# Optimization experiments

Hardware: AMD Instinct MI355X
Metric: run time of the kernel (lower is better)

## Reference

```python
import jax, jax.numpy as jnp
import numpy as np

B, L, C, H, W = 4, 16, 64, 64, 64
F, NH, NB = 128, 2, 2


def _ln(x, w, b, eps=1e-5):
    # LayerNorm over last two dims (H, W), torch-style biased variance
    m = jnp.mean(x, axis=(-2, -1), keepdims=True)
    v = jnp.var(x, axis=(-2, -1), keepdims=True)
    return (x - m) * jax.lax.rsqrt(v + eps) * w + b


def _conv2d(x, w, b):
    # x: (N, Cin, H, W), w: (Cout, Cin, k, k) -- the (1,k,k) Conv3d acts per-frame
    y = jax.lax.conv_general_dilated(x, w, (1, 1), 'SAME',
                                     dimension_numbers=('NCHW', 'OIHW', 'NCHW'))
    return y + b[None, :, None, None]


def _combine(c1, c2):
    a1, b1 = c1
    a2, b2 = c2
    return a1 * a2, a2 * b1 + b2


def _forward(x, params_log, pBw_r, pBw_i, pBb_r, pBb_i, pCw_r, pCw_i, pCb_r, pCb_i,
             lru_ln_w, lru_ln_b, cin_w, cin_b, h3_w, h3_b, h1_w, h1_b,
             h_ln_w, h_ln_b, cout_w, cout_b, ffn_ln_w, ffn_ln_b):
    gelu = lambda t: jax.nn.gelu(t, approximate=False)
    Bsz, Ln, Cc, Hh, Ww = x.shape
    for i in range(NB):
        # ---- ConvLRULayer ----
        pl = params_log[i]
        nu = jnp.exp(pl[:Cc])            # (C, H)
        theta = jnp.exp(pl[Cc:2 * Cc])   # (C, H)
        gamma = jnp.exp(pl[2 * Cc:])     # (C, H)
        lamb = jnp.exp(jax.lax.complex(-nu, theta))  # (C, H) complex
        Bw = jax.lax.complex(pBw_r[i], pBw_i[i])
        Bb = jax.lax.complex(pBb_r[i], pBb_i[i])
        Cw = jax.lax.complex(pCw_r[i], pCw_i[i])
        Cb = jax.lax.complex(pCb_r[i], pCb_i[i])
        h = jnp.fft.fft2(x.astype(jnp.complex64), axes=(-2, -1))  # (B,L,C,H,W)
        h = jnp.einsum('blchw,oc->blohw', h, Bw) + Bb[None, None, :, None, None]
        h = h * gamma[None, None, :, :, None]
        # parallel scan: h[t] = lamb * h[t-1] + h[t] along L
        a = jnp.broadcast_to(lamb[None, None, :, :, None], (Bsz, Ln, Cc, Hh, 1))
        _, h = jax.lax.associative_scan(_combine, (a, h), axis=1)
        h = jnp.fft.ifft2(h, axes=(-2, -1))
        h = jnp.einsum('blchw,oc->blohw', h, Cw) + Cb[None, None, :, None, None]
        h = _ln(h.real, lru_ln_w[i], lru_ln_b[i])
        x = h + x
        # ---- FeedForward (all Conv3d have kernel 1 in L -> per-frame 2D) ----
        y = x.reshape(Bsz * Ln, Cc, Hh, Ww)
        y_ = gelu(_conv2d(y, cin_w[i], cin_b[i]))  # (B*L, F, H, W)
        for j in range(NH):
            t = gelu(_conv2d(y_, h3_w[i, j], h3_b[i, j]))
            t = gelu(jnp.einsum('nfhw,of->nohw', t, h1_w[i, j])
                     + h1_b[i, j][None, :, None, None])
            y_ = _ln(t, h_ln_w[i, j], h_ln_b[i, j]) + y_
        t = jnp.einsum('nfhw,of->nohw', y_, cout_w[i]) + cout_b[i][None, :, None, None]
        t = _ln(t, ffn_ln_w[i], ffn_ln_b[i])
        x = t.reshape(Bsz, Ln, Cc, Hh, Ww) + x
    return x


def setup_inputs() -> dict:
    key = jax.random.key(0)
    ks = jax.random.split(key, 16)
    x = jax.random.normal(ks[0], (B, L, C, H, W), jnp.float32)
    # LRU stability init (as in the torch module)
    r_min, r_max = 0.8, 0.99
    u1 = jax.random.uniform(ks[1], (NB, C, H), jnp.float32)
    u2 = jax.random.uniform(ks[2], (NB, C, H), jnp.float32)
    nu_log = jnp.log(-0.5 * jnp.log(u1 * (r_max ** 2 - r_min ** 2) + r_min ** 2))
    theta_log = jnp.log(u2 * 2.0 * np.pi)
    gamma_log = 0.5 * jnp.log(1.0 - jnp.exp(-2.0 * jnp.exp(nu_log)))
    params_log = jnp.concatenate([nu_log, theta_log, gamma_log], axis=1)  # (NB, 3C, H)

    def nrm(k, shape, fan_in):
        return jax.random.normal(k, shape, jnp.float32) / np.sqrt(fan_in)

    return dict(
        x=x, params_log=params_log,
        pBw_r=nrm(ks[3], (NB, C, C), C), pBw_i=jnp.zeros((NB, C, C), jnp.float32),
        pBb_r=jnp.zeros((NB, C), jnp.float32), pBb_i=jnp.zeros((NB, C), jnp.float32),
        pCw_r=nrm(ks[4], (NB, C, C), C), pCw_i=jnp.zeros((NB, C, C), jnp.float32),
        pCb_r=jnp.zeros((NB, C), jnp.float32), pCb_i=jnp.zeros((NB, C), jnp.float32),
        lru_ln_w=jnp.ones((NB, H, W), jnp.float32), lru_ln_b=jnp.zeros((NB, H, W), jnp.float32),
        cin_w=nrm(ks[5], (NB, F, C, 7, 7), C * 49), cin_b=jnp.zeros((NB, F), jnp.float32),
        h3_w=nrm(ks[6], (NB, NH, F, F, 3, 3), F * 9), h3_b=jnp.zeros((NB, NH, F), jnp.float32),
        h1_w=nrm(ks[7], (NB, NH, F, F), F), h1_b=jnp.zeros((NB, NH, F), jnp.float32),
        h_ln_w=jnp.ones((NB, NH, H, W), jnp.float32), h_ln_b=jnp.zeros((NB, NH, H, W), jnp.float32),
        cout_w=nrm(ks[8], (NB, C, F), F), cout_b=jnp.zeros((NB, C), jnp.float32),
        ffn_ln_w=jnp.ones((NB, H, W), jnp.float32), ffn_ln_b=jnp.zeros((NB, H, W), jnp.float32),
    )


def reference(x, params_log, pBw_r, pBw_i, pBb_r, pBb_i, pCw_r, pCw_i, pCb_r, pCb_i,
              lru_ln_w, lru_ln_b, cin_w, cin_b, h3_w, h3_b, h1_w, h1_b,
              h_ln_w, h_ln_b, cout_w, cout_b, ffn_ln_w, ffn_ln_b):
    return _forward(x, params_log, pBw_r, pBw_i, pBb_r, pBb_i, pCw_r, pCw_i,
                    pCb_r, pCb_i, lru_ln_w, lru_ln_b, cin_w, cin_b, h3_w, h3_b,
                    h1_w, h1_b, h_ln_w, h_ln_b, cout_w, cout_b, ffn_ln_w, ffn_ln_b)
```

## Files before the change

### kernel.cpp

```cpp
#include <hip/hip_runtime.h>
#include <math.h>

static constexpr int Bd = 4, Ld = 16, Cd = 64, Hd = 64, Wd = 64, Fd = 128;
static constexpr int NBLK = 2, NHEAD = 2;
static constexpr int HW = 4096;
static constexpr float TWO_PI = 6.28318530717958647692f;

typedef __attribute__((ext_vector_type(8))) short bf16x8;
typedef __attribute__((ext_vector_type(4))) float f32x4;
typedef __attribute__((ext_vector_type(4))) unsigned int u32x4;

__device__ __forceinline__ float gelu_f(float v) {
    float x2 = v * v;
    float u = v * (0.797884560802865f + 0.0356774081363f * x2);
    float au = fabsf(u);
    float e = __expf(-2.f * au);
    float th = (1.f - e) * __builtin_amdgcn_rcpf(1.f + e);
    th = copysignf(th, u);
    return 0.5f * v * (1.f + th);
}

__device__ __forceinline__ unsigned short bf16c(float f) {
    unsigned int u = __float_as_uint(f);
    unsigned int r = (u + 0x7fffu + ((u >> 16) & 1u)) >> 16;
    return (unsigned short)r;
}
__device__ __forceinline__ float bf2f(unsigned short u) {
    return __uint_as_float((unsigned int)u << 16);
}
__device__ __forceinline__ unsigned int packbf(float r, float i) {
    return (unsigned int)bf16c(r) | ((unsigned int)bf16c(i) << 16);
}
__device__ __forceinline__ bf16x8 bneg(bf16x8 v) {
    u32x4 u = *(u32x4*)&v;
    u = u ^ 0x80008000u;
    return *(bf16x8*)&u;
}

__device__ __forceinline__ void gl2lds16(const void* g, void* l) {
    __builtin_amdgcn_global_load_lds(
        (const __attribute__((address_space(1))) void*)g,
        (__attribute__((address_space(3))) void*)l, 16, 0, 0);
}

__global__ void k_prepdft(unsigned short* __restrict__ o) {
    int idx = blockIdx.x * 256 + threadIdx.x;
    if (idx >= 16384) return;
    int sec = idx >> 12, j = idx & 4095;
    int a = j >> 6, b = j & 63;
    float ang = (TWO_PI / 64.f) * (float)((a * b) & 63);
    float sv, cv;
    __sincosf(ang, &sv, &cv);
    float v;
    if (sec == 0) v = cv;
    else if (sec == 1) v = -sv;
    else if (sec == 2) v = cv * (1.f / 64.f);
    else v = -sv * (1.f / 64.f);
    o[idx] = bf16c(v);
}

__global__ void k_preplru(const float* __restrict__ bwr, const float* __restrict__ bwi,
                          const float* __restrict__ cwr, const float* __restrict__ cwi,
                          const float* __restrict__ gl,
                          unsigned short* __restrict__ wout, float* __restrict__ gamT) {
    int idx = blockIdx.x * 256 + threadIdx.x;
    if (idx < 16384) {
        int sec = idx >> 12, j = idx & 4095;
        const float* s = (sec == 0) ? bwr : (sec == 1) ? bwi : (sec == 2) ? cwr : cwi;
        wout[idx] = bf16c(s[j]);
    } else if (idx < 20480) {
        int j = idx - 16384;
        int fh = j >> 6, o2 = j & 63;
        gamT[j] = __expf(gl[o2 * 64 + fh]);
    }
}

__global__ __launch_bounds__(256) void k_dfthm(const float* __restrict__ x,
                                               unsigned int* __restrict__ X,
                                               const unsigned short* __restrict__ tcb,
                                               const unsigned short* __restrict__ tsb) {
    __shared__ __align__(16) unsigned char smm[49152];
    unsigned char* xpT = smm;
    unsigned char* tC = smm + 32768;
    unsigned char* tS = smm + 40960;
    int blk = blockIdx.x;
    int fi = blk >> 4;
    int w0 = (blk & 15) * 4;
    int t = threadIdx.x, lane = t & 63, wv = t >> 6;
    int pl = lane & 15, kg = lane >> 4;
    int l3 = lane >> 3, l7 = lane & 7;

    for (int q = 0; q < 2; ++q) {
        int sg = q * 4 + wv;
        gl2lds16(tcb + (size_t)(sg * 8 + l3) * 64 + (l7 ^ l3) * 8, tC + sg * 1024);
        gl2lds16(tsb + (size_t)(sg * 8 + l3) * 64 + (l7 ^ l3) * 8, tS + sg * 1024);
    }
    const float* xf = x + (size_t)fi * Cd * HW;
    int h = t & 63;
    for (int k = 0; k < 16; ++k) {
        int c = k * 4 + (t >> 6);
        float4 v = *(const float4*)(xf + (size_t)c * HW + h * 64 + w0);
        float vv[4] = {v.x, v.y, v.z, v.w};
#pragma unroll
        for (int q = 0; q < 4; ++q) {
            int pos = q * 64 + c;
            *(unsigned short*)(xpT + pos * 128 + ((h * 2) ^ ((c & 7) << 4))) = bf16c(vv[q]);
        }
    }
    __syncthreads();

    int w = w0 + wv;
    unsigned int* Xw = X + (size_t)fi * 262144 + (size_t)w * 4096;
    for (int half = 0; half < 2; ++half) {
        f32x4 aR[2][4], aI[2][4];
#pragma unroll
        for (int mt = 0; mt < 2; ++mt)
#pragma unroll
            for (int nt = 0; nt < 4; ++nt) { aR[mt][nt] = (f32x4)0.f; aI[mt][nt] = (f32x4)0.f; }
#pragma unroll
        for (int ks = 0; ks < 2; ++ks) {
            int koff = (ks * 64 + kg * 16);
            bf16x8 ac[2], as_[2], b[4];
#pragma unroll
            for (int mt = 0; mt < 2; ++mt) {
                int row = half * 32 + mt * 16 + pl;
                int off = row * 128 + (koff ^ ((pl & 7) << 4));
                ac[mt] = *(const bf16x8*)(tC + off);
                as_[mt] = *(const bf16x8*)(tS + off);
            }
#pragma unroll
            for (int nt = 0; nt < 4; ++nt) {
                int pos = wv * 64 + nt * 16 + pl;
                b[nt] = *(const bf16x8*)(xpT + pos * 128 + (koff ^ ((pl & 7) << 4)));
            }
#pragma unroll
            for (int mt = 0; mt < 2; ++mt)
#pragma unroll
                for (int nt = 0; nt < 4; ++nt) {
                    aR[mt][nt] = __builtin_amdgcn_mfma_f32_16x16x32_bf16(ac[mt], b[nt], aR[mt][nt], 0, 0, 0);
                    aI[mt][nt] = __builtin_amdgcn_mfma_f32_16x16x32_bf16(as_[mt], b[nt], aI[mt][nt], 0, 0, 0);
                }
        }
#pragma unroll
        for (int mt = 0; mt < 2; ++mt)
#pragma unroll
            for (int nt = 0; nt < 4; ++nt) {
                int c = nt * 16 + pl;
#pragma unroll
                for (int r = 0; r < 4; ++r) {
                    int fh = half * 32 + mt * 16 + kg * 4 + r;
                    Xw[fh * 64 + c] = packbf(aR[mt][nt][r], aI[mt][nt][r]);
                }
            }
    }
}

__global__ __launch_bounds__(256) void k_lrumid(unsigned int* __restrict__ X,
                                                const unsigned short* __restrict__ wbr,
                                                const unsigned short* __restrict__ wbi,
                                                const unsigned short* __restrict__ wcr,
                                                const unsigned short* __restrict__ wci,
                                                const float* __restrict__ gamT,
                                                const float* __restrict__ br_g,
                                                const float* __restrict__ bi_g,
                                                const float* __restrict__ plg) {
    __shared__ __align__(16) unsigned char smm[81920];
    unsigned char* inr = smm;
    unsigned char* ini = smm + 8192;
    unsigned char* hre = smm + 16384;
    unsigned char* him = smm + 24576;
    unsigned char* wBR = smm + 32768;
    unsigned char* wBI = smm + 40960;
    unsigned char* wCR = smm + 49152;
    unsigned char* wCI = smm + 57344;
    float* gam = (float*)(smm + 65536);
    int blk = blockIdx.x;
    int b = blk >> 6, s = blk & 63;
    int t = threadIdx.x, lane = t & 63, wv = t >> 6;
    int pj = lane & 15, kg = lane >> 4;
    int l3 = lane >> 3, l7 = lane & 7;

    for (int q = 0; q < 2; ++q) {
        int sg = q * 4 + wv;
        size_t goff = (size_t)(sg * 8 + l3) * 64 + (l7 ^ l3) * 8;
        gl2lds16(wbr + goff, wBR + sg * 1024);
        gl2lds16(wbi + goff, wBI + sg * 1024);
        gl2lds16(wcr + goff, wCR + sg * 1024);
        gl2lds16(wci + goff, wCI + sg * 1024);
    }
    for (int j = t; j < 4096; j += 256) gam[j] = gamT[j];

    float lamr[4][4], lami[4][4];
#pragma unroll
    for (int nt = 0; nt < 4; ++nt) {
        int o = nt * 16 + pj;
#pragma unroll
        for (int r = 0; r < 4; ++r) {
            int fh = wv * 16 + kg * 4 + r;
            float nu = expf(plg[o * 64 + fh]);
            float th = expf(plg[4096 + o * 64 + fh]);
            float mag = expf(-nu);
            float sth, cth;
            sincosf(th, &sth, &cth);
            lamr[nt][r] = mag * cth;
            lami[nt][r] = mag * sth;
        }
    }
    float bRo[4], bIo[4];
#pragma unroll
    for (int nt = 0; nt < 4; ++nt) {
        bRo[nt] = (s == 0) ? br_g[nt * 16 + pj] : 0.f;
        bIo[nt] = (s == 0) ? bi_g[nt * 16 + pj] : 0.f;
    }
    float str[4][4], sti[4][4];
    unsigned int* Xfrm = X + (size_t)b * 16 * 262144 + (size_t)s * 4096;

    for (int l = 0; l < 16; ++l) {
        unsigned int* Xi = Xfrm + (size_t)l * 262144;
        __syncthreads();
        for (int k = 0; k < 4; ++k) {
            int j = k * 256 + t;
            int row = j >> 4, c0 = (j & 15) * 4;
            u32x4 v = *(const u32x4*)(Xi + (size_t)row * 64 + c0);
            unsigned int rw0 = (v.x & 0xffffu) | (v.y << 16);
            unsigned int rw1 = (v.z & 0xffffu) | (v.w << 16);
            unsigned int iw0 = (v.x >> 16) | (v.y & 0xffff0000u);
            unsigned int iw1 = (v.z >> 16) | (v.w & 0xffff0000u);
            int off = row * 128 + ((((c0 >> 3) ^ (row & 7)) << 4) | ((c0 & 7) * 2));
            *(unsigned int*)(inr + off) = rw0;
            *(unsigned int*)(inr + off + 4) = rw1;
            *(unsigned int*)(ini + off) = iw0;
            *(unsigned int*)(ini + off + 4) = iw1;
        }
        __syncthreads();

        f32x4 cR[4], cI[4];
#pragma unroll
        for (int nt = 0; nt < 4; ++nt) { cR[nt] = (f32x4)0.f; cI[nt] = (f32x4)0.f; }
#pragma unroll
        for (int ks = 0; ks < 2; ++ks) {
            int koff = ks * 64 + kg * 16;
            int aoff = (wv * 16 + pj) * 128 + (koff ^ ((pj & 7) << 4));
            bf16x8 ar = *(const bf16x8*)(inr + aoff);
            bf16x8 ai = *(const bf16x8*)(ini + aoff);
            bf16x8 an = bneg(ai);
#pragma unroll
            for (int nt = 0; nt < 4; ++nt) {
                int o = nt * 16 + pj;
                int woff = o * 128 + (koff ^ ((pj & 7) << 4));
                bf16x8 brf = *(const bf16x8*)(wBR + woff);
                bf16x8 bif = *(const bf16x8*)(wBI + woff);
                cR[nt] = __builtin_amdgcn_mfma_f32_16x16x32_bf16(ar, brf, cR[nt], 0, 0, 0);
                cR[nt] = __builtin_amdgcn_mfma_f32_16x16x32_bf16(an, bif, cR[nt], 0, 0, 0);
                cI[nt] = __builtin_amdgcn_mfma_f32_16x16x32_bf16(ar, bif, cI[nt], 0, 0, 0);
                cI[nt] = __builtin_amdgcn_mfma_f32_16x16x32_bf16(ai, brf, cI[nt], 0, 0, 0);
            }
        }
#pragma unroll
        for (int nt = 0; nt < 4; ++nt) {
            int o = nt * 16 + pj;
#pragma unroll
            for (int r = 0; r < 4; ++r) {
                int row = wv * 16 + kg * 4 + r;
                float g = gam[row * 64 + o];
                float vr = (cR[nt][r] + bRo[nt]) * g;
                float vi = (cI[nt][r] + bIo[nt]) * g;
                if (l == 0) {
                    str[nt][r] = vr;
                    sti[nt][r] = vi;
                } else {
                    float nr = lamr[nt][r] * str[nt][r] - lami[nt][r] * sti[nt][r] + vr;
                    float ni = lamr[nt][r] * sti[nt][r] + lami[nt][r] * str[nt][r] + vi;
                    str[nt][r] = nr;
                    sti[nt][r] = ni;
                }
                int hoff = row * 128 + ((((o >> 3) ^ (row & 7)) << 4) | ((o & 7) * 2));
                *(unsigned short*)(hre + hoff) = bf16c(str[nt][r]);
                *(unsigned short*)(him + hoff) = bf16c(sti[nt][r]);
            }
        }
        __syncthreads();

        f32x4 dR[4], dI[4];
#pragma unroll
        for (int nt = 0; nt < 4; ++nt) { dR[nt] = (f32x4)0.f; dI[nt] = (f32x4)0.f; }
#pragma unroll
        for (int ks = 0; ks < 2; ++ks) {
            int koff = ks * 64 + kg * 16;
            int aoff = (wv * 16 + pj) * 128 + (koff ^ ((pj & 7) << 4));
            bf16x8 ar = *(const bf16x8*)(hre + aoff);
            bf16x8 ai = *(const bf16x8*)(him + aoff);
            bf16x8 an = bneg(ai);
#pragma unroll
            for (int nt = 0; nt < 4; ++nt) {
                int o = nt * 16 + pj;
                int woff = o * 128 + (koff ^ ((pj & 7) << 4));
                bf16x8 brf = *(const bf16x8*)(wCR + woff);
                bf16x8 bif = *(const bf16x8*)(wCI + woff);
                dR[nt] = __builtin_amdgcn_mfma_f32_16x16x32_bf16(ar, brf, dR[nt], 0, 0, 0);
                dR[nt] = __builtin_amdgcn_mfma_f32_16x16x32_bf16(an, bif, dR[nt], 0, 0, 0);
                dI[nt] = __builtin_amdgcn_mfma_f32_16x16x32_bf16(ar, bif, dI[nt], 0, 0, 0);
                dI[nt] = __builtin_amdgcn_mfma_f32_16x16x32_bf16(ai, brf, dI[nt], 0, 0, 0);
            }
        }
#pragma unroll
        for (int nt = 0; nt < 4; ++nt) {
            int o = nt * 16 + pj;
#pragma unroll
            for (int r = 0; r < 4; ++r) {
                int row = wv * 16 + kg * 4 + r;
                Xi[(size_t)row * 64 + o] = packbf(dR[nt][r], dI[nt][r]);
            }
        }
    }
}

__global__ __launch_bounds__(256) void k_idfthm_ln(const unsigned int* __restrict__ X,
                                                   const unsigned short* __restrict__ tic,
                                                   const unsigned short* __restrict__ tis,
                                                   const float* __restrict__ cbr,
                                                   const float* __restrict__ lnw,
                                                   const float* __restrict__ lnb,
                                                   const float* __restrict__ xprev,
                                                   float* __restrict__ xout) {
    __shared__ __align__(16) unsigned char smm[81920];
    unsigned char* SrT = smm;
    unsigned char* SiT = smm + 32768;
    unsigned char* tC = smm + 65536;
    unsigned char* tS = smm + 73728;
    float* y4 = (float*)smm;
    int blk = blockIdx.x;
    int fi = blk >> 4;
    int c0 = (blk & 15) * 4;
    int t = threadIdx.x, lane = t & 63, wv = t >> 6;
    int pl = lane & 15, kg = lane >> 4;
    int l3 = lane >> 3, l7 = lane & 7;

    for (int q = 0; q < 2; ++q) {
        int sg = q * 4 + wv;
        gl2lds16(tic + (size_t)(sg * 8 + l3) * 64 + (l7 ^ l3) * 8, tC + sg * 1024);
        gl2lds16(tis + (size_t)(sg * 8 + l3) * 64 + (l7 ^ l3) * 8, tS + sg * 1024);
    }
    const unsigned int* Xf = X + (size_t)fi * 262144;
    int fh = t & 63;
    for (int k = 0; k < 16; ++k) {
        int w = k * 4 + (t >> 6);
        u32x4 v = *(const u32x4*)(Xf + (size_t)w * 4096 + fh * 64 + c0);
        unsigned int vv[4] = {v.x, v.y, v.z, v.w};
#pragma unroll
        for (int cj = 0; cj < 4; ++cj) {
            int pos2 = w * 4 + cj;
            int off = pos2 * 128 + ((fh * 2) ^ ((pos2 & 7) << 4));
            *(unsigned short*)(SrT + off) = (unsigned short)(vv[cj] & 0xffffu);
            *(unsigned short*)(SiT + off) = (unsigned short)(vv[cj] >> 16);
        }
    }
    __syncthreads();

    f32x4 y[4][4];
#pragma unroll
    for (int mt = 0; mt < 4; ++mt)
#pragma unroll
        for (int nt = 0; nt < 4; ++nt) y[mt][nt] = (f32x4)0.f;
#pragma unroll
    for (int ks = 0; ks < 2; ++ks) {
        int koff = ks * 64 + kg * 16;
        bf16x8 ac[4], as_[4], brf[4], bif[4];
#pragma unroll
        for (int mt = 0; mt < 4; ++mt) {
            int row = mt * 16 + pl;
            int off = row * 128 + (koff ^ ((pl & 7) << 4));
            ac[mt] = *(const bf16x8*)(tC + off);
            as_[mt] = *(const bf16x8*)(tS + off);
        }
#pragma unroll
        for (int nt = 0; nt < 4; ++nt) {
            int pos2 = wv * 64 + nt * 16 + pl;
            int off = pos2 * 128 + (koff ^ ((pl & 7) << 4));
            brf[nt] = *(const bf16x8*)(SrT + off);
            bif[nt] = *(const bf16x8*)(SiT + off);
        }
#pragma unroll
        for (int mt = 0; mt < 4; ++mt)
#pragma unroll
            for (int nt = 0; nt < 4; ++nt) {
                y[mt][nt] = __builtin_amdgcn_mfma_f32_16x16x32_bf16(ac[mt], brf[nt], y[mt][nt], 0, 0, 0);
                y[mt][nt] = __builtin_amdgcn_mfma_f32_16x16x32_bf16(as_[mt], bif[nt], y[mt][nt], 0, 0, 0);
            }
    }
    __syncthreads();

    float cb4[4];
#pragma unroll
    for (int cj = 0; cj < 4; ++cj) cb4[cj] = cbr[c0 + cj];
#pragma unroll
    for (int mt = 0; mt < 4; ++mt)
#pragma unroll
        for (int nt = 0; nt < 4; ++nt) {
            int pos2 = wv * 64 + nt * 16 + pl;
            int w = pos2 >> 2, cj = pos2 & 3;
#pragma unroll
            for (int r = 0; r < 4; ++r) {
                int h = mt * 16 + kg * 4 + r;
                y4[cj * 4232 + h * 66 + w] = y[mt][nt][r] + cb4[cj];
            }
        }
    __syncthreads();

    int w = lane;
    const float* yp = y4 + wv * 4232;
    float s = 0.f, q = 0.f;
    for (int h = 0; h < 64; ++h) {
        float v = yp[h * 66 + w];
        s += v;
        q += v * v;
    }
#pragma unroll
    for (int off = 32; off; off >>= 1) {
        s += __shfl_xor(s, off);
        q += __shfl_xor(q, off);
    }
    float m = s * (1.f / 4096.f);
    float var = q * (1.f / 4096.f) - m * m;
    float rs = rsqrtf(var + 1e-5f);
    int c = c0 + wv;
    const float* xp = xprev + ((size_t)fi * Cd + c) * HW;
    float* xo = xout + ((size_t)fi * Cd + c) * HW;
    for (int h = 0; h < 64; ++h) {
        int p = h * 64 + w;
        xo[p] = (yp[h * 66 + w] - m) * rs * lnw[p] + lnb[p] + xp[p];
    }
}

__global__ __launch_bounds__(256) void k_ln_res(const unsigned short* __restrict__ t_in,
                                                const float* __restrict__ w,
                                                const float* __restrict__ b,
                                                float* __restrict__ dst) {
    __shared__ float red[8];
    int fr = blockIdx.x;
    int t = threadIdx.x;
    const unsigned short* src = t_in + (size_t)fr * HW + t * 16;
    float* d = dst + (size_t)fr * HW + t * 16;
    u32x4 v0 = *(const u32x4*)(src);
    u32x4 v1 = *(const u32x4*)(src + 8);
    float vals[16];
    unsigned int vw[8] = {v0.x, v0.y, v0.z, v0.w, v1.x, v1.y, v1.z, v1.w};
#pragma unroll
    for (int j = 0; j < 8; ++j) {
        vals[j * 2] = bf2f((unsigned short)(vw[j] & 0xffffu));
        vals[j * 2 + 1] = bf2f((unsigned short)(vw[j] >> 16));
    }
    float s = 0.f, sq = 0.f;
#pragma unroll
    for (int j = 0; j < 16; ++j) { s += vals[j]; sq += vals[j] * vals[j]; }
    for (int off = 32; off; off >>= 1) {
        s += __shfl_down(s, off);
        sq += __shfl_down(sq, off);
    }
    int wid = t >> 6;
    if ((t & 63) == 0) { red[wid] = s; red[4 + wid] = sq; }
    __syncthreads();
    s = red[0] + red[1] + red[2] + red[3];
    sq = red[4] + red[5] + red[6] + red[7];
    float m = s * (1.f / 4096.f);
    float var = sq * (1.f / 4096.f) - m * m;
    float rs = rsqrtf(var + 1e-5f);
    const float* wp = w + t * 16;
    const float* bp = b + t * 16;
#pragma unroll
    for (int q4 = 0; q4 < 4; ++q4) {
        float4 wv4 = *(const float4*)(wp + q4 * 4);
        float4 bv4 = *(const float4*)(bp + q4 * 4);
        float4 dv = *(const float4*)(d + q4 * 4);
        dv.x += (vals[q4 * 4 + 0] - m) * rs * wv4.x + bv4.x;
        dv.y += (vals[q4 * 4 + 1] - m) * rs * wv4.y + bv4.y;
        dv.z += (vals[q4 * 4 + 2] - m) * rs * wv4.z + bv4.z;
        dv.w += (vals[q4 * 4 + 3] - m) * rs * wv4.w + bv4.w;
        *(float4*)(d + q4 * 4) = dv;
    }
}

__global__ void k_prep7(const float* __restrict__ w, unsigned short* __restrict__ o) {
    int idx = blockIdx.x * 256 + threadIdx.x;
    if (idx < 49 * 128 * 64) {
        int tap = idx >> 13, rem = idx & 8191, f = rem >> 6, c = rem & 63;
        o[idx] = bf16c(w[(size_t)(f * 64 + c) * 49 + tap]);
    }
}
__global__ void k_prep3(const float* __restrict__ w, unsigned short* __restrict__ o,
                        int nh) {
    int idx = blockIdx.x * 256 + threadIdx.x;
    if (idx < nh * 147456) {
        int head = idx / 147456;
        int rem = idx - head * 147456;
        int tap = rem >> 14, r2 = rem & 16383, f = r2 >> 7, c = r2 & 127;
        o[idx] = bf16c(w[(size_t)head * 147456 + (size_t)(f * 128 + c) * 9 + tap]);
    }
}
__global__ void k_prepcvt(const float* __restrict__ w, unsigned short* __restrict__ o, int n) {
    int idx = blockIdx.x * 256 + threadIdx.x;
    if (idx < n) o[idx] = bf16c(w[idx]);
}

__global__ __launch_bounds__(256) void k_t2p(const float* __restrict__ x,
                                             unsigned short* __restrict__ xT) {
    __shared__ float tile[64][65];
    int blk = blockIdx.x;
    int f = blk >> 6;
    int p0 = (blk & 63) * 64;
    int t = threadIdx.x;
    const float* src = x + (size_t)f * Cd * HW;
    for (int j = t; j < 4096; j += 256) {
        int c = j >> 6, p = j & 63;
        tile[c][p] = src[(size_t)c * HW + p0 + p];
    }
    __syncthreads();
    unsigned short* dst = xT + ((size_t)f * HW + p0) * 64;
    for (int j = t; j < 4096; j += 256) {
        int p = j >> 6, c = j & 63;
        dst[(size_t)p * 64 + c] = bf16c(tile[c][p]);
    }
}

__global__ __launch_bounds__(512) void k_conv7m(const unsigned short* __restrict__ xT,
                                                const unsigned short* __restrict__ wb,
                                                const float* __restrict__ bias,
                                                unsigned short* __restrict__ yout) {
    __shared__ __align__(16) unsigned char smm[158208];
    unsigned char* inT = smm;
    unsigned char* wt0 = smm + 125440;
    int blk = blockIdx.x;
    int fi = blk >> 3;
    int y0 = (blk & 7) * 8;
    int t = threadIdx.x, lane = t & 63, wv = t >> 6;
    int l3 = lane >> 3, l7 = lane & 7;

    const unsigned short* xf = xT + (size_t)fi * HW * 64;
    float4 z4 = make_float4(0.f, 0.f, 0.f, 0.f);
    int ksw_in = l7 ^ ((3 + l3) & 7);
    for (int idx = wv; idx < 112; idx += 8) {
        int r = idx >> 3, sg = idx & 7;
        int srow = y0 + r - 3;
        unsigned char* dst = inT + r * 8960 + 3 * 128 + sg * 1024;
        if (srow >= 0 && srow < 64) {
            gl2lds16(xf + (size_t)srow * 4096 + (sg * 8 + l3) * 64 + ksw_in * 8, dst);
        } else {
            *(float4*)(dst + lane * 16) = z4;
        }
    }
    for (int j = t; j < 672; j += 512) {
        int r = j / 48, k = j % 48;
        int xp = (k < 24) ? (k >> 3) : 67 + ((k - 24) >> 3);
        *(float4*)(inT + r * 8960 + xp * 128 + (k & 7) * 16) = z4;
    }
    int ksw_w = l7 ^ l3;
    for (int q = 0; q < 2; ++q) {
        int sg = q * 8 + wv;
        int f = sg * 8 + l3;
        gl2lds16(wb + (size_t)f * 64 + ksw_w * 8, wt0 + sg * 1024);
    }
    __syncthreads();

    int wm = wv & 3, wn = wv >> 2;
    f32x4 acc[8][4];
#pragma unroll
    for (int m = 0; m < 8; ++m)
#pragma unroll
        for (int n = 0; n < 4; ++n) acc[m][n] = (f32x4)0.f;
    int kg = lane >> 4, pl = lane & 15;
    int cur = 0;
    for (int tap = 0; tap < 49; ++tap) {
        if (tap + 1 < 49) {
            const unsigned short* g = wb + (size_t)(tap + 1) * 8192;
            unsigned char* wdst = wt0 + (cur ^ 1) * 16384;
            for (int q = 0; q < 2; ++q) {
                int sg = q * 8 + wv;
                int f = sg * 8 + l3;
                gl2lds16(g + (size_t)f * 64 + ksw_w * 8, wdst + sg * 1024);
            }
        }
        unsigned char* wcur = wt0 + cur * 16384;
        int ky = tap / 7, kx = tap % 7;
#pragma unroll
        for (int ks = 0; ks < 2; ++ks) {
            bf16x8 a[8], b[4];
#pragma unroll
            for (int m = 0; m < 8; ++m) {
                int row = wm * 2 + (m >> 2) + ky;
                int xp = (m & 3) * 16 + pl + kx;
                a[m] = *(const bf16x8*)(inT + row * 8960 + xp * 128 +
                                        (((ks * 4 + kg) ^ (xp & 7)) << 4));
            }
#pragma unroll
            for (int n = 0; n < 4; ++n) {
                int rowf = wn * 64 + n * 16 + pl;
                b[n] = *(const bf16x8*)(wcur + rowf * 128 +
                                        (((ks * 4 + kg) ^ (pl & 7)) << 4));
            }
#pragma unroll
            for (int m = 0; m < 8; ++m)
#pragma unroll
                for (int n = 0; n < 4; ++n)
                    acc[m][n] = __builtin_amdgcn_mfma_f32_16x16x32_bf16(a[m], b[n], acc[m][n], 0, 0, 0);
        }
        __syncthreads();
        cur ^= 1;
    }
    unsigned short* yo = yout + ((size_t)fi * HW + (size_t)y0 * 64) * 128;
#pragma unroll
    for (int m = 0; m < 8; ++m) {
        int rowl = wm * 2 + (m >> 2);
#pragma unroll
        for (int n = 0; n < 4; ++n) {
            int f = wn * 64 + n * 16 + pl;
            float bs = bias[f];
#pragma unroll
            for (int r = 0; r < 4; ++r) {
                int x = (m & 3) * 16 + kg * 4 + r;
                yo[(size_t)(rowl * 64 + x) * 128 + f] = bf16c(gelu_f(acc[m][n][r] + bs));
            }
        }
    }
}

__global__ __launch_bounds__(512) void k_conv3f(const unsigned short* __restrict__ yin,
                                                const unsigned short* __restrict__ wb,
                                                const float* __restrict__ bias3,
                                                const unsigned short* __restrict__ w1,
                                                const float* __restrict__ bias1,
                                                unsigned short* __restrict__ outp2,
                                                float* __restrict__ lnpart) {
    __shared__ __align__(16) unsigned char smm[134144];
    __shared__ float redS[8][64], redQ[8][64];
    unsigned char* inT = smm;
    unsigned char* wL = smm + 101376;
    int blk = blockIdx.x;
    int fi = blk >> 4;
    int y0 = (blk & 15) * 4;
    int t = threadIdx.x, lane = t & 63, wv = t >> 6;
    int l4 = lane >> 4, l15 = lane & 15;
    const unsigned short* yf = yin + (size_t)fi * HW * 128;
    float4 z4 = make_float4(0.f, 0.f, 0.f, 0.f);
    for (int seg = wv; seg < 96; seg += 8) {
        int r = seg >> 4, xs = seg & 15;
        int srow = y0 + r - 1;
        int xp = 1 + xs * 4 + l4;
        unsigned char* dst = inT + r * 16896 + (size_t)(1 + xs * 4) * 256;
        if (srow >= 0 && srow < 64) {
            int gsrc = l15 ^ (xp & 7);
            gl2lds16(yf + ((size_t)(srow * 64 + xp - 1) * 128 + gsrc * 8), dst);
        } else {
            *(float4*)(dst + lane * 16) = z4;
        }
    }
    if (t < 192) {
        int r = t / 32, k = t & 31;
        int xp = (k < 16) ? 0 : 65;
        *(float4*)(inT + r * 16896 + xp * 256 + (k & 15) * 16) = z4;
    }
    for (int sg = wv; sg < 32; sg += 8) {
        int f = sg * 4 + l4;
        gl2lds16(wb + (size_t)f * 128 + (l15 ^ (f & 7)) * 8, wL + sg * 1024);
    }
    __syncthreads();

    int wm = wv & 3, wn = wv >> 2;
    f32x4 acc[4][4];
#pragma unroll
    for (int m = 0; m < 4; ++m)
#pragma unroll
        for (int n = 0; n < 4; ++n) acc[m][n] = (f32x4)0.f;
    int kg = lane >> 4, pl = lane & 15;
    int fw = t >> 2, qw = t & 3;
    u32x4 rg[4];
    for (int tap = 0; tap < 9; ++tap) {
        if (tap < 8) {
            const u32x4* src = (const u32x4*)(wb + (size_t)(tap + 1) * 16384 +
                                              (size_t)fw * 128 + qw * 32);
#pragma unroll
            for (int j = 0; j < 4; ++j) rg[j] = src[j];
        }
        int ky = tap / 3, kx = tap % 3;
        int rbase = (wm + ky) * 16896;
#pragma unroll
        for (int ks = 0; ks < 4; ++ks) {
            bf16x8 a[4], b[4];
#pragma unroll
            for (int m = 0; m < 4; ++m) {
                int xp = m * 16 + pl + kx;
                a[m] = *(const bf16x8*)(inT + rbase + (size_t)xp * 256 +
                                        ((ks * 64 + kg * 16) ^ ((xp & 7) << 4)));
            }
#pragma unroll
            for (int n = 0; n < 4; ++n) {
                int row = wn * 64 + n * 16 + pl;
                b[n] = *(const bf16x8*)(wL + (size_t)row * 256 +
                                        ((ks * 64 + kg * 16) ^ ((pl & 7) << 4)));
            }
#pragma unroll
            for (int m = 0; m < 4; ++m)
#pragma unroll
                for (int n = 0; n < 4; ++n)
                    acc[m][n] = __builtin_amdgcn_mfma_f32_16x16x32_bf16(a[m], b[n], acc[m][n], 0, 0, 0);
        }
        __syncthreads();
        if (tap < 8) {
#pragma unroll
            for (int j = 0; j < 4; ++j)
                *(u32x4*)(wL + (size_t)fw * 256 + (((qw * 4 + j) ^ (fw & 7)) << 4)) = rg[j];
        }
        __syncthreads();
    }

    unsigned char* tL = smm;
    unsigned char* w1L = smm + 65536;
#pragma unroll
    for (int m = 0; m < 4; ++m)
#pragma unroll
        for (int n = 0; n < 4; ++n) {
            int f = wn * 64 + n * 16 + pl;
            float bs = bias3[f];
#pragma unroll
            for (int r = 0; r < 4; ++r) {
                int pos = wm * 64 + m * 16 + kg * 4 + r;
                *(unsigned short*)(tL + (size_t)pos * 256 +
                    ((((f >> 3) ^ (pos & 7)) << 4) | ((f & 7) * 2))) =
                    bf16c(gelu_f(acc[m][n][r] + bs));
            }
        }
    for (int sg = wv; sg < 32; sg += 8) {
        int rr = sg * 4 + l4;
        gl2lds16(w1 + (size_t)rr * 128 + (l15 ^ (rr & 7)) * 8, w1L + sg * 1024);
    }
    __syncthreads();

    f32x4 fa[4][4];
#pragma unroll
    for (int m = 0; m < 4; ++m)
#pragma unroll
        for (int n = 0; n < 4; ++n) fa[m][n] = (f32x4)0.f;
#pragma unroll
    for (int ks = 0; ks < 4; ++ks) {
        bf16x8 a[4], b[4];
#pragma unroll
        for (int m = 0; m < 4; ++m) {
            int row = wm * 64 + m * 16 + pl;
            a[m] = *(const bf16x8*)(tL + (size_t)row * 256 +
                                    ((ks * 64 + kg * 16) ^ ((pl & 7) << 4)));
        }
#pragma unroll
        for (int n = 0; n < 4; ++n) {
            int row = wn * 64 + n * 16 + pl;
            b[n] = *(const bf16x8*)(w1L + (size_t)row * 256 +
                                    ((ks * 64 + kg * 16) ^ ((pl & 7) << 4)));
        }
#pragma unroll
        for (int m = 0; m < 4; ++m)
#pragma unroll
            for (int n = 0; n < 4; ++n)
                fa[m][n] = __builtin_amdgcn_mfma_f32_16x16x32_bf16(a[m], b[n], fa[m][n], 0, 0, 0);
    }
    __syncthreads();

    int slab = blk & 15;
    int p0 = slab * 256;
    unsigned char* oL = smm;
#pragma unroll
    for (int n = 0; n < 4; ++n) {
        int f = wn * 64 + n * 16 + pl;
        float bs = bias1[f];
        float s = 0.f, q = 0.f;
#pragma unroll
        for (int m = 0; m < 4; ++m)
#pragma unroll
            for (int r = 0; r < 4; ++r) {
                float v = gelu_f(fa[m][n][r] + bs);
                int pos = wm * 64 + m * 16 + kg * 4 + r;
                *(unsigned short*)(oL + (size_t)pos * 256 +
                    ((((f >> 3) ^ (pos & 7)) << 4) | ((f & 7) * 2))) = bf16c(v);
                s += v;
                q += v * v;
            }
        s += __shfl_xor(s, 16); s += __shfl_xor(s, 32);
        q += __shfl_xor(q, 16); q += __shfl_xor(q, 32);
        if (kg == 0) { redS[wv][n * 16 + pl] = s; redQ[wv][n * 16 + pl] = q; }
    }
    __syncthreads();
    unsigned char* o0 = (unsigned char*)(outp2 + ((size_t)fi * HW + p0) * 128);
#pragma unroll
    for (int it = 0; it < 8; ++it) {
        int gid = it * 512 + t;
        int pos = gid >> 4, g = gid & 15;
        u32x4 v = *(const u32x4*)(oL + (size_t)pos * 256 + ((g ^ (pos & 7)) << 4));
        *(u32x4*)(o0 + (size_t)pos * 256 + g * 16) = v;
    }
    if (t < 128) {
        int wh = t >> 6, j = t & 63;
        float s = redS[wh * 4][j] + redS[wh * 4 + 1][j] + redS[wh * 4 + 2][j] + redS[wh * 4 + 3][j];
        float q = redQ[wh * 4][j] + redQ[wh * 4 + 1][j] + redQ[wh * 4 + 2][j] + redQ[wh * 4 + 3][j];
        float* lp = lnpart + ((size_t)(fi * 16 + slab) * 128 + t) * 2;
        lp[0] = s;
        lp[1] = q;
    }
}

__global__ __launch_bounds__(256) void k_lnapply2(const unsigned short* __restrict__ t2,
                                                  const float* __restrict__ lnpart,
                                                  const float* __restrict__ w,
                                                  const float* __restrict__ b,
                                                  unsigned short* __restrict__ y) {
    __shared__ float sm_m[128], sm_r[128];
    int blk = blockIdx.x;
    int fi = blk >> 5, p0 = (blk & 31) * 128;
    int t = threadIdx.x;
    if (t < 128) {
        float s = 0.f, q = 0.f;
        for (int sl = 0; sl < 16; ++sl) {
            const float* lp = lnpart + ((size_t)(fi * 16 + sl) * 128 + t) * 2;
            s += lp[0];
            q += lp[1];
        }
        float m = s * (1.f / 4096.f);
        float var = q * (1.f / 4096.f) - m * m;
        sm_m[t] = m;
        sm_r[t] = rsqrtf(var + 1e-5f);
    }
    __syncthreads();
    int f = t & 127, ph = t >> 7;
    for (int k = ph; k < 128; k += 2) {
        int p = p0 + k;
        size_t idx = ((size_t)fi * HW + p) * 128 + f;
        float v = bf2f(t2[idx]);
        float yv = bf2f(y[idx]);
        y[idx] = bf16c(yv + (v - sm_m[f]) * sm_r[f] * w[p] + b[p]);
    }
}

__global__ __launch_bounds__(256) void k_coutm(const unsigned short* __restrict__ yin,
                                               const unsigned short* __restrict__ wt,
                                               const float* __restrict__ bias,
                                               unsigned short* __restrict__ outp) {
    __shared__ __align__(16) unsigned char smm[49152];
    unsigned char* inL = smm;
    unsigned char* wL = smm + 32768;
    int blk = blockIdx.x;
    int fi = blk >> 5;
    int p0 = (blk & 31) * 128;
    int t = threadIdx.x, lane = t & 63, wv = t >> 6;
    int l4 = lane >> 4, l15 = lane & 15;
    for (int sg = wv; sg < 16; sg += 4) {
        int r = sg * 4 + l4;
        gl2lds16(wt + (size_t)r * 128 + (l15 ^ (r & 7)) * 8, wL + sg * 1024);
    }
    const unsigned short* yb = yin + (size_t)fi * HW * 128;
    for (int sg = wv; sg < 32; sg += 4) {
        int pos = sg * 4 + l4;
        gl2lds16(yb + ((size_t)(p0 + pos) * 128 + (l15 ^ (pos & 7)) * 8), inL + sg * 1024);
    }
    __syncthreads();
    int wm = wv & 1, wn = wv >> 1;
    f32x4 acc[2][4];
#pragma unroll
    for (int m = 0; m < 2; ++m)
#pragma unroll
        for (int n = 0; n < 4; ++n) acc[m][n] = (f32x4)0.f;
    int kg = lane >> 4, pl = lane & 15;
#pragma unroll
    for (int ks = 0; ks < 4; ++ks) {
        bf16x8 a[2], b[4];
#pragma unroll
        for (int m = 0; m < 2; ++m) {
            int row = wm * 32 + m * 16 + pl;
            a[m] = *(const bf16x8*)(wL + (size_t)row * 256 +
                                    ((ks * 64 + kg * 16) ^ ((pl & 7) << 4)));
        }
#pragma unroll
        for (int n = 0; n < 4; ++n) {
            int row = wn * 64 + n * 16 + pl;
            b[n] = *(const bf16x8*)(inL + (size_t)row * 256 +
                                    ((ks * 64 + kg * 16) ^ ((pl & 7) << 4)));
        }
#pragma unroll
        for (int m = 0; m < 2; ++m)
#pragma unroll
            for (int n = 0; n < 4; ++n)
                acc[m][n] = __builtin_amdgcn_mfma_f32_16x16x32_bf16(a[m], b[n], acc[m][n], 0, 0, 0);
    }
    __syncthreads();
    unsigned char* oL = smm;
#pragma unroll
    for (int m = 0; m < 2; ++m)
#pragma unroll
        for (int n = 0; n < 4; ++n) {
            int posl = wn * 64 + n * 16 + pl;
#pragma unroll
            for (int r = 0; r < 4; ++r) {
                int c = wm * 32 + m * 16 + kg * 4 + r;
                *(unsigned short*)(oL + (size_t)c * 256 +
                    ((((posl >> 3) ^ (c & 7)) << 4) | ((posl & 7) * 2))) =
                    bf16c(acc[m][n][r] + bias[c]);
            }
        }
    __syncthreads();
#pragma unroll
    for (int it = 0; it < 4; ++it) {
        int gid = it * 256 + t;
        int c = gid >> 4, g = gid & 15;
        u32x4 v = *(const u32x4*)(oL + (size_t)c * 256 + ((g ^ (c & 7)) << 4));
        *(u32x4*)((unsigned char*)(outp + ((size_t)fi * 64 + c) * HW + p0) + g * 16) = v;
    }
}

extern "C" void kernel_launch(void* const* d_in, const int* in_sizes, int n_in,
                              void* d_out, int out_size, void* d_ws, size_t ws_size,
                              hipStream_t stream) {
    (void)in_sizes; (void)n_in; (void)out_size;
    const float* x_in  = (const float*)d_in[0];
    const float* pl    = (const float*)d_in[1];
    const float* pBw_r = (const float*)d_in[2];
    const float* pBw_i = (const float*)d_in[3];
    const float* pBb_r = (const float*)d_in[4];
    const float* pBb_i = (const float*)d_in[5];
    const float* pCw_r = (const float*)d_in[6];
    const float* pCw_i = (const float*)d_in[7];
    const float* pCb_r = (const float*)d_in[8];
    const float* pCb_i = (const float*)d_in[9];
    const float* lruw  = (const float*)d_in[10];
    const float* lrub  = (const float*)d_in[11];
    const float* cinw  = (const float*)d_in[12];
    const float* cinb  = (const float*)d_in[13];
    const float* h3w   = (const float*)d_in[14];
    const float* h3b   = (const float*)d_in[15];
    const float* h1w   = (const float*)d_in[16];
    const float* h1b   = (const float*)d_in[17];
    const float* hlnw  = (const float*)d_in[18];
    const float* hlnb  = (const float*)d_in[19];
    const float* coutw = (const float*)d_in[20];
    const float* coutb = (const float*)d_in[21];
    const float* flnw  = (const float*)d_in[22];
    const float* flnb  = (const float*)d_in[23];
    float* out = (float*)d_out;

    int FR = 8, LB = 1;
    {
        const int frs[6] = {64, 32, 16, 16, 8, 8};
        const int lbs[6] = {4, 4, 4, 2, 2, 1};
        for (int k = 0; k < 6; ++k) {
            size_t region = (size_t)lbs[k] * 16777216ULL;
            size_t ffn = (size_t)frs[k] * 3145728ULL;
            if (ffn > region) region = ffn;
            size_t needb = region + 1605632ULL + (size_t)frs[k] * 32768ULL + 65536ULL;
            if (needb <= ws_size) { FR = frs[k]; LB = lbs[k]; break; }
        }
    }
    size_t region = (size_t)LB * 16777216ULL;
    {
        size_t ffn = (size_t)FR * 3145728ULL;
        if (ffn > region) region = ffn;
    }
    unsigned char* ws = (unsigned char*)d_ws;
    unsigned int* Xb = (unsigned int*)ws;
    unsigned short* ybuf = (unsigned short*)ws;
    unsigned short* t2bf = (unsigned short*)(ws + (size_t)FR * 1048576);
    unsigned short* xT   = (unsigned short*)(ws + (size_t)FR * 2097152);
    unsigned short* cobuf = (unsigned short*)(ws + (size_t)FR * 2621440);
    unsigned char* wbase = ws + region;
    unsigned short* wb7  = (unsigned short*)(wbase);
    unsigned short* wb3  = (unsigned short*)(wbase + 802816);
    unsigned short* wb1  = (unsigned short*)(wbase + 1392640);
    unsigned short* wbco = (unsigned short*)(wbase + 1458176);
    unsigned short* dftT = (unsigned short*)(wbase + 1474560);
    unsigned short* lruW = (unsigned short*)(wbase + 1507328);
    float* gamT          = (float*)(wbase + 1540096);
    float* lnpart        = (float*)(wbase + 1556480);
    unsigned short* tcb = dftT;
    unsigned short* tsb = dftT + 4096;
    unsigned short* tic = dftT + 8192;
    unsigned short* tis = dftT + 12288;
    unsigned short* wBr = lruW;
    unsigned short* wBi = lruW + 4096;
    unsigned short* wCr = lruW + 8192;
    unsigned short* wCi = lruW + 12288;

    const int NCl = 4 / LB;
    const int NCf = 64 / FR;

    k_prepdft<<<64, 256, 0, stream>>>(dftT);

    for (int i = 0; i < NBLK; ++i) {
        const float* xsrc = (i == 0) ? x_in : out;

        k_preplru<<<80, 256, 0, stream>>>(pBw_r + (size_t)i * 4096,
                                          pBw_i + (size_t)i * 4096,
                                          pCw_r + (size_t)i * 4096,
                                          pCw_i + (size_t)i * 4096,
                                          pl + (size_t)i * 12288 + 8192, lruW, gamT);
        for (int cc = 0; cc < NCl; ++cc) {
            size_t boff = (size_t)cc * LB * 4194304;
            k_dfthm<<<LB * 256, 256, 0, stream>>>(xsrc + boff, Xb, tcb, tsb);
            k_lrumid<<<LB * 64, 256, 0, stream>>>(Xb, wBr, wBi, wCr, wCi, gamT,
                                                  pBb_r + (size_t)i * 64,
                                                  pBb_i + (size_t)i * 64,
                                                  pl + (size_t)i * 12288);
            k_idfthm_ln<<<LB * 256, 256, 0, stream>>>(Xb, tic, tis,
                                                      pCb_r + (size_t)i * 64,
                                                      lruw + (size_t)i * 4096,
                                                      lrub + (size_t)i * 4096,
                                                      xsrc + boff, out + boff);
        }

        k_prep7<<<1568, 256, 0, stream>>>(cinw + (size_t)i * 401408, wb7);
        k_prep3<<<1152, 256, 0, stream>>>(h3w + (size_t)i * 2 * 147456, wb3, 2);
        k_prepcvt<<<128, 256, 0, stream>>>(h1w + (size_t)i * 2 * 16384, wb1, 32768);
        k_prepcvt<<<32, 256, 0, stream>>>(coutw + (size_t)i * 8192, wbco, 8192);

        for (int cc = 0; cc < NCf; ++cc) {
            float* xb = out + (size_t)cc * FR * 262144;
            k_t2p<<<FR * 64, 256, 0, stream>>>(xb, xT);
            k_conv7m<<<FR * 8, 512, 0, stream>>>(xT, wb7, cinb + (size_t)i * 128, ybuf);
            for (int j = 0; j < NHEAD; ++j) {
                k_conv3f<<<FR * 16, 512, 0, stream>>>(ybuf, wb3 + (size_t)j * 147456,
                                                      h3b + (size_t)(i * 2 + j) * 128,
                                                      wb1 + (size_t)j * 16384,
                                                      h1b + (size_t)(i * 2 + j) * 128,
                                                      t2bf, lnpart);
                k_lnapply2<<<FR * 32, 256, 0, stream>>>(t2bf, lnpart,
                                                        hlnw + (size_t)(i * 2 + j) * 4096,
                                                        hlnb + (size_t)(i * 2 + j) * 4096,
                                                        ybuf);
            }
            k_coutm<<<FR * 32, 256, 0, stream>>>(ybuf, wbco, coutb + (size_t)i * 64, cobuf);
            k_ln_res<<<FR * 64, 256, 0, stream>>>(cobuf, flnw + (size_t)i * 4096,
                                                  flnb + (size_t)i * 4096, xb);
        }
    }
}
```

Measured before the change: 1.648 ms.

## Double-buffer conv3x3 tap weights in LDS via async global-to-LDS loads

Replaces the register-staged per-tap weight reload in the fused 3x3 conv kernel with two LDS weight buffers. The next tap's weights are loaded directly global-to-LDS while the current tap computes, which removes one barrier per tap. The input tile drops its padding columns: edge columns are clamped and zeroed in registers instead. LDS use grows to 160KB, which may limit occupancy, and the reduction arrays are moved into the shared buffer.

```diff
diff --git a/kernel.cpp b/kernel.cpp
--- a/kernel.cpp
+++ b/kernel.cpp
@@ -630,10 +630,9 @@
                                                 const float* __restrict__ bias1,
                                                 unsigned short* __restrict__ outp2,
                                                 float* __restrict__ lnpart) {
-    __shared__ __align__(16) unsigned char smm[134144];
-    __shared__ float redS[8][64], redQ[8][64];
+    __shared__ __align__(16) unsigned char smm[163840];
     unsigned char* inT = smm;
-    unsigned char* wL = smm + 101376;
+    unsigned char* wt0 = smm + 98304;
     int blk = blockIdx.x;
     int fi = blk >> 4;
     int y0 = (blk & 15) * 4;
@@ -644,23 +643,19 @@
     for (int seg = wv; seg < 96; seg += 8) {
         int r = seg >> 4, xs = seg & 15;
         int srow = y0 + r - 1;
-        int xp = 1 + xs * 4 + l4;
-        unsigned char* dst = inT + r * 16896 + (size_t)(1 + xs * 4) * 256;
+        int col = xs * 4 + l4;
+        unsigned char* dst = inT + r * 16384 + xs * 4 * 256;
         if (srow >= 0 && srow < 64) {
-            int gsrc = l15 ^ (xp & 7);
-            gl2lds16(yf + ((size_t)(srow * 64 + xp - 1) * 128 + gsrc * 8), dst);
+            int gs = l15 ^ (col & 7);
+            gl2lds16(yf + ((size_t)(srow * 64 + col) * 128 + gs * 8), dst);
         } else {
             *(float4*)(dst + lane * 16) = z4;
         }
     }
-    if (t < 192) {
-        int r = t / 32, k = t & 31;
-        int xp = (k < 16) ? 0 : 65;
-        *(float4*)(inT + r * 16896 + xp * 256 + (k & 15) * 16) = z4;
-    }
-    for (int sg = wv; sg < 32; sg += 8) {
+    for (int q = 0; q < 4; ++q) {
+        int sg = q * 8 + wv;
         int f = sg * 4 + l4;
-        gl2lds16(wb + (size_t)f * 128 + (l15 ^ (f & 7)) * 8, wL + sg * 1024);
+        gl2lds16(wb + (size_t)f * 128 + (l15 ^ (f & 7)) * 8, wt0 + sg * 1024);
     }
     __syncthreads();
 
@@ -671,30 +666,40 @@
 #pragma unroll
         for (int n = 0; n < 4; ++n) acc[m][n] = (f32x4)0.f;
     int kg = lane >> 4, pl = lane & 15;
-    int fw = t >> 2, qw = t & 3;
-    u32x4 rg[4];
+    bf16x8 z8 = (bf16x8)(short)0;
+    int cur = 0;
+#pragma unroll
     for (int tap = 0; tap < 9; ++tap) {
-        if (tap < 8) {
-            const u32x4* src = (const u32x4*)(wb + (size_t)(tap + 1) * 16384 +
-                                              (size_t)fw * 128 + qw * 32);
-#pragma unroll
-            for (int j = 0; j < 4; ++j) rg[j] = src[j];
-        }
-        int ky = tap / 3, kx = tap % 3;
-        int rbase = (wm + ky) * 16896;
+        if (tap + 1 < 9) {
+            const unsigned short* g = wb + (size_t)(tap + 1) * 16384;
+            unsigned char* wdst = wt0 + (cur ^ 1) * 32768;
+            for (int q = 0; q < 4; ++q) {
+                int sg = q * 8 + wv;
+                int f = sg * 4 + l4;
+                gl2lds16(g + (size_t)f * 128 + (l15 ^ (f & 7)) * 8, wdst + sg * 1024);
+            }
+        }
+        unsigned char* wcur = wt0 + cur * 32768;
+        const int ky = tap / 3, kx = tap % 3;
+        int rbase = (wm + ky) * 16384;
 #pragma unroll
         for (int ks = 0; ks < 4; ++ks) {
             bf16x8 a[4], b[4];
 #pragma unroll
             for (int m = 0; m < 4; ++m) {
-                int xp = m * 16 + pl + kx;
-                a[m] = *(const bf16x8*)(inT + rbase + (size_t)xp * 256 +
-                                        ((ks * 64 + kg * 16) ^ ((xp & 7) << 4)));
+                int col = m * 16 + pl + kx - 1;
+                int colc = col;
+                if (kx == 0 && m == 0) colc = (col < 0) ? 0 : col;
+                if (kx == 2 && m == 3) colc = (col > 63) ? 63 : col;
+                a[m] = *(const bf16x8*)(inT + rbase + colc * 256 +
+                                        ((ks * 64 + kg * 16) ^ ((colc & 7) << 4)));
+                if (kx == 0 && m == 0) a[m] = (pl == 0) ? z8 : a[m];
+                if (kx == 2 && m == 3) a[m] = (pl == 15) ? z8 : a[m];
             }
 #pragma unroll
             for (int n = 0; n < 4; ++n) {
                 int row = wn * 64 + n * 16 + pl;
-                b[n] = *(const bf16x8*)(wL + (size_t)row * 256 +
+                b[n] = *(const bf16x8*)(wcur + (size_t)row * 256 +
                                         ((ks * 64 + kg * 16) ^ ((pl & 7) << 4)));
             }
 #pragma unroll
@@ -704,16 +709,13 @@
                     acc[m][n] = __builtin_amdgcn_mfma_f32_16x16x32_bf16(a[m], b[n], acc[m][n], 0, 0, 0);
         }
         __syncthreads();
-        if (tap < 8) {
-#pragma unroll
-            for (int j = 0; j < 4; ++j)
-                *(u32x4*)(wL + (size_t)fw * 256 + (((qw * 4 + j) ^ (fw & 7)) << 4)) = rg[j];
-        }
-        __syncthreads();
+        cur ^= 1;
     }
 
     unsigned char* tL = smm;
     unsigned char* w1L = smm + 65536;
+    float (*redS)[64] = (float (*)[64])(smm + 155648);
+    float (*redQ)[64] = (float (*)[64])(smm + 157696);
 #pragma unroll
     for (int m = 0; m < 4; ++m)
 #pragma unroll
```

Result: no change. 1.630 ms (-1.1%).
